# Optimization experiments

Measured on AMD Instinct MI355X. Metric: run time of the kernel, lower is better.

The kernel has to match this reference:

```python
import jax, jax.numpy as jnp
import numpy as np

N_NODES = 50000
N_EDGES = 800000
N_GRAPHS = 64
NEG_SLOPE = 0.2
EPS = 1e-16


def _gat_layer(x, src, dst, W, b, att_l, att_r):
    H, C = att_l.shape
    n = x.shape[0]
    # lin_l == lin_r (shared weights in the source module)
    xl = (x @ W.T + b).reshape(n, H, C)            # [N,H,C]
    alpha_l = jnp.sum(xl * att_l, axis=-1)         # [N,H]
    alpha_r = jnp.sum(xl * att_r, axis=-1)         # [N,H]
    # per-edge attention logits: alpha_i (dst) + alpha_j (src)
    e = jax.nn.leaky_relu(alpha_r[dst] + alpha_l[src], NEG_SLOPE)  # [E,H]
    # segment softmax over destination node
    m = jax.ops.segment_max(e, dst, num_segments=n)
    e = jnp.exp(e - m[dst])
    denom = jax.ops.segment_sum(e, dst, num_segments=n)
    alpha = e / (denom[dst] + EPS)                 # [E,H]
    msg = xl[src] * alpha[:, :, None]              # [E,H,C]
    out = jax.ops.segment_sum(msg, dst, num_segments=n)  # [N,H,C]
    return out.reshape(n, H * C)


def setup_inputs() -> dict:
    key = jax.random.key(0)
    ks = jax.random.split(key, 10)
    x = jax.random.normal(ks[0], (N_NODES, 128), dtype=jnp.float32)
    edge_index = jax.random.randint(ks[1], (2, N_EDGES), 0, N_NODES, dtype=jnp.int32)
    batch = jnp.sort(jax.random.randint(ks[2], (N_NODES,), 0, N_GRAPHS, dtype=jnp.int32))
    s = 1.0 / np.sqrt(128.0)
    Ws = jax.random.normal(ks[3], (3, 128, 128), dtype=jnp.float32) * s
    bs = jnp.zeros((3, 128), dtype=jnp.float32)
    att_ls = jax.random.normal(ks[4], (3, 4, 32), dtype=jnp.float32) * s
    att_rs = jax.random.normal(ks[5], (3, 4, 32), dtype=jnp.float32) * s
    proj_W = jax.random.normal(ks[6], (32, 128), dtype=jnp.float32) * s
    proj_b = jnp.zeros((32,), dtype=jnp.float32)
    return {"x": x, "edge_index": edge_index, "batch": batch, "Ws": Ws, "bs": bs,
            "att_ls": att_ls, "att_rs": att_rs, "proj_W": proj_W, "proj_b": proj_b}


def reference(x, edge_index, batch, Ws, bs, att_ls, att_rs, proj_W, proj_b):
    src, dst = edge_index[0], edge_index[1]
    h = x
    for l in range(3):
        h = _gat_layer(h, src, dst, Ws[l], bs[l], att_ls[l], att_rs[l])
        h = jax.nn.relu(h)  # dropout disabled (eval mode)
    pooled = jax.ops.segment_sum(h, batch, num_segments=N_GRAPHS)  # [G, H*C]
    return pooled @ proj_W.T + proj_b  # output_dim=None -> return embedding
```

## Files before the change

kernel.cpp:

```cpp
#include <hip/hip_runtime.h>
#include <hip/hip_bf16.h>

#define NHEADS 4
#define DIM 128
#define NEG_SLOPE 0.2f
#define POOL_CHUNK 256

typedef __bf16 bf16x8 __attribute__((ext_vector_type(8)));
typedef float  f32x4  __attribute__((ext_vector_type(4)));

__device__ __forceinline__ float lrelu(float x) { return x > 0.f ? x : NEG_SLOPE * x; }
__device__ __forceinline__ float bf2f(unsigned short u) {
    return __uint_as_float(((unsigned)u) << 16);
}
__device__ __forceinline__ unsigned short f2bf(float f) {
    __bf16 b = (__bf16)f;
    return __builtin_bit_cast(unsigned short, b);
}
__device__ __forceinline__ float4 lrelu4(float4 a, float4 b) {
    return make_float4(lrelu(a.x + b.x), lrelu(a.y + b.y), lrelu(a.z + b.z), lrelu(a.w + b.w));
}
__device__ __forceinline__ float4 redmax4(float4 v) {
#pragma unroll
    for (int off = 32; off >= 1; off >>= 1) {
        v.x = fmaxf(v.x, __shfl_xor(v.x, off));
        v.y = fmaxf(v.y, __shfl_xor(v.y, off));
        v.z = fmaxf(v.z, __shfl_xor(v.z, off));
        v.w = fmaxf(v.w, __shfl_xor(v.w, off));
    }
    return v;
}
__device__ __forceinline__ float4 redsum4(float4 v) {
#pragma unroll
    for (int off = 32; off >= 1; off >>= 1) {
        v.x += __shfl_xor(v.x, off);
        v.y += __shfl_xor(v.y, off);
        v.z += __shfl_xor(v.z, off);
        v.w += __shfl_xor(v.w, off);
    }
    return v;
}

__global__ __launch_bounds__(256) void pack_w(
    const float* __restrict__ Ws, __bf16* __restrict__ Wb, int total)
{
    int o = blockIdx.x * 256 + threadIdx.x;
    if (o >= total) return;
    int layer = o >> 14;
    int t = o & 16383;
    int j = t & 7, l = (t >> 3) & 63, kk = (t >> 9) & 3, g = t >> 11;
    int col = g * 16 + (l & 15);
    int k = kk * 32 + (l >> 4) * 8 + j;
    Wb[o] = (__bf16)Ws[(size_t)layer * 16384 + col * 128 + k];
}

template<bool ABF>
__device__ __forceinline__ void gemm_body(
    const float* __restrict__ inF, const unsigned short* __restrict__ inB,
    const uint4* __restrict__ Wb4, const float* __restrict__ bias,
    const float* __restrict__ attl, const float* __restrict__ attr,
    __bf16* __restrict__ xlb, float* __restrict__ al, float* __restrict__ ar,
    int n, int bid)
{
    const int tid = threadIdx.x;
    const int wid = tid >> 6, l = tid & 63;
    const int rowA = bid * 64 + wid * 16 + (l & 15);
    const int kchunk = (l >> 4) * 8;

    f32x4 acc[8];
#pragma unroll
    for (int g = 0; g < 8; ++g)
#pragma unroll
        for (int r = 0; r < 4; ++r) acc[g][r] = 0.f;

#pragma unroll
    for (int kk = 0; kk < 4; ++kk) {
        bf16x8 afrag;
        if (ABF) {
            uint4 u = make_uint4(0, 0, 0, 0);
            if (rowA < n)
                u = *(const uint4*)(inB + (size_t)rowA * DIM + kk * 32 + kchunk);
            afrag = __builtin_bit_cast(bf16x8, u);
        } else {
            float av[8];
            if (rowA < n) {
                const float* p = inF + (size_t)rowA * DIM + kk * 32 + kchunk;
                float4 x0 = *(const float4*)p;
                float4 x1 = *(const float4*)(p + 4);
                av[0]=x0.x; av[1]=x0.y; av[2]=x0.z; av[3]=x0.w;
                av[4]=x1.x; av[5]=x1.y; av[6]=x1.z; av[7]=x1.w;
            } else {
#pragma unroll
                for (int i = 0; i < 8; ++i) av[i] = 0.f;
            }
#pragma unroll
            for (int i = 0; i < 8; ++i) afrag[i] = (__bf16)av[i];
        }
#pragma unroll
        for (int g = 0; g < 8; ++g) {
            uint4 u = Wb4[(g * 4 + kk) * 64 + l];
            bf16x8 bfrag = __builtin_bit_cast(bf16x8, u);
            acc[g] = __builtin_amdgcn_mfma_f32_16x16x32_bf16(afrag, bfrag, acc[g], 0, 0, 0);
        }
    }

    const int rowbase = bid * 64 + wid * 16 + (l >> 4) * 4;
    float pl[4][4], pr2[4][4];
#pragma unroll
    for (int r = 0; r < 4; ++r)
#pragma unroll
        for (int h = 0; h < 4; ++h) { pl[r][h] = 0.f; pr2[r][h] = 0.f; }

#pragma unroll
    for (int g = 0; g < 8; ++g) {
        int col = g * 16 + (l & 15);
        float bg = bias[col], alg = attl[col], arg = attr[col];
        int h = g >> 1;
#pragma unroll
        for (int r = 0; r < 4; ++r) {
            float v = acc[g][r] + bg;
            int row = rowbase + r;
            if (row < n) xlb[(size_t)row * DIM + col] = (__bf16)v;
            pl[r][h]  = fmaf(v, alg, pl[r][h]);
            pr2[r][h] = fmaf(v, arg, pr2[r][h]);
        }
    }
#pragma unroll
    for (int off = 1; off <= 8; off <<= 1) {
#pragma unroll
        for (int r = 0; r < 4; ++r)
#pragma unroll
            for (int h = 0; h < 4; ++h) {
                pl[r][h]  += __shfl_xor(pl[r][h], off);
                pr2[r][h] += __shfl_xor(pr2[r][h], off);
            }
    }
    if ((l & 15) == 0) {
#pragma unroll
        for (int r = 0; r < 4; ++r) {
            int row = rowbase + r;
            if (row < n) {
#pragma unroll
                for (int h = 0; h < 4; ++h) {
                    al[row * 4 + h] = pl[r][h];
                    ar[row * 4 + h] = pr2[r][h];
                }
            }
        }
    }
}

template<bool ABF>
__global__ __launch_bounds__(256) void gemm_mfma(
    const float* __restrict__ inF, const unsigned short* __restrict__ inB,
    const uint4* __restrict__ Wb4, const float* __restrict__ bias,
    const float* __restrict__ attl, const float* __restrict__ attr,
    __bf16* __restrict__ xlb, float* __restrict__ al, float* __restrict__ ar, int n)
{
    gemm_body<ABF>(inF, inB, Wb4, bias, attl, attr, xlb, al, ar, n, blockIdx.x);
}

__global__ __launch_bounds__(256) void gemm0_scatter(
    const float* __restrict__ inF, const uint4* __restrict__ Wb4,
    const float* __restrict__ bias,
    const float* __restrict__ attl, const float* __restrict__ attr,
    __bf16* __restrict__ xlb, float* __restrict__ al, float* __restrict__ ar,
    int n, int gemmBlocks,
    const int* __restrict__ src, const int* __restrict__ dst,
    int* __restrict__ wpos, int* __restrict__ col, int E)
{
    if ((int)blockIdx.x < gemmBlocks) {
        gemm_body<false>(inF, nullptr, Wb4, bias, attl, attr, xlb, al, ar, n, blockIdx.x);
    } else {
        int e = (blockIdx.x - gemmBlocks) * 256 + threadIdx.x;
        if (e < E) {
            int p = atomicAdd(&wpos[dst[e]], 1);
            col[p] = src[e];
        }
    }
}

__global__ __launch_bounds__(256) void deg_count(
    const int* __restrict__ dst, int* __restrict__ deg, int E)
{
    int e = blockIdx.x * blockDim.x + threadIdx.x;
    if (e < E) atomicAdd(&deg[dst[e]], 1);
}

__global__ __launch_bounds__(256) void scan_blocks(
    const int* __restrict__ deg, int* __restrict__ rowptr,
    int* __restrict__ partials, int n)
{
    __shared__ int tot[256];
    int t = threadIdx.x;
    int base = blockIdx.x * 1024 + t * 4;
    int v[4];
#pragma unroll
    for (int j = 0; j < 4; ++j) v[j] = (base + j < n) ? deg[base + j] : 0;
    int p1 = v[0], p2 = p1 + v[1], p3 = p2 + v[2], sum4 = p3 + v[3];
    tot[t] = sum4;
    __syncthreads();
    int val = sum4;
    for (int off = 1; off < 256; off <<= 1) {
        int other = (t >= off) ? tot[t - off] : 0;
        __syncthreads();
        val += other;
        tot[t] = val;
        __syncthreads();
    }
    int excl = val - sum4;
    if (base < n)     rowptr[base]     = excl;
    if (base+1 < n)   rowptr[base+1]   = excl + p1;
    if (base+2 < n)   rowptr[base+2]   = excl + p2;
    if (base+3 < n)   rowptr[base+3]   = excl + p3;
    if (t == 255) partials[blockIdx.x] = val;
}

__global__ __launch_bounds__(256) void scan_partials(
    int* __restrict__ partials, int nb, int* __restrict__ rowptr, int n)
{
    __shared__ int tot[256];
    int t = threadIdx.x;
    int v = (t < nb) ? partials[t] : 0;
    tot[t] = v;
    __syncthreads();
    int val = v;
    for (int off = 1; off < 256; off <<= 1) {
        int other = (t >= off) ? tot[t - off] : 0;
        __syncthreads();
        val += other;
        tot[t] = val;
        __syncthreads();
    }
    if (t < nb) partials[t] = val - v;
    if (t == 255) rowptr[n] = val;
}

__global__ __launch_bounds__(256) void add_offsets(
    int* __restrict__ rowptr, int* __restrict__ wpos,
    const int* __restrict__ partials, int n)
{
    int base = blockIdx.x * 1024 + threadIdx.x * 4;
    int off = partials[blockIdx.x];
#pragma unroll
    for (int j = 0; j < 4; ++j) {
        int i = base + j;
        if (i < n) { int r = rowptr[i] + off; rowptr[i] = r; wpos[i] = r; }
    }
}

__device__ __forceinline__ void agg_chunk2(
    const int* __restrict__ slds, const float* __restrict__ wl,
    int cn, int q, const unsigned short* __restrict__ xp,
    f32x4& A, f32x4& B, f32x4& C, f32x4& D)
{
    int i = 0;
    for (; i + 8 <= cn; i += 8) {
        int e0 = i + q, e1 = i + 2 + q, e2 = i + 4 + q, e3 = i + 6 + q;
        int s0 = slds[e0], s1 = slds[e1], s2 = slds[e2], s3 = slds[e3];
        float w0 = wl[e0*4], w1 = wl[e1*4], w2 = wl[e2*4], w3 = wl[e3*4];
        ushort4 v0 = *(const ushort4*)(xp + (size_t)s0 * DIM);
        ushort4 v1 = *(const ushort4*)(xp + (size_t)s1 * DIM);
        ushort4 v2 = *(const ushort4*)(xp + (size_t)s2 * DIM);
        ushort4 v3 = *(const ushort4*)(xp + (size_t)s3 * DIM);
        A[0] = fmaf(w0, bf2f(v0.x), A[0]); A[1] = fmaf(w0, bf2f(v0.y), A[1]);
        A[2] = fmaf(w0, bf2f(v0.z), A[2]); A[3] = fmaf(w0, bf2f(v0.w), A[3]);
        B[0] = fmaf(w1, bf2f(v1.x), B[0]); B[1] = fmaf(w1, bf2f(v1.y), B[1]);
        B[2] = fmaf(w1, bf2f(v1.z), B[2]); B[3] = fmaf(w1, bf2f(v1.w), B[3]);
        C[0] = fmaf(w2, bf2f(v2.x), C[0]); C[1] = fmaf(w2, bf2f(v2.y), C[1]);
        C[2] = fmaf(w2, bf2f(v2.z), C[2]); C[3] = fmaf(w2, bf2f(v2.w), C[3]);
        D[0] = fmaf(w3, bf2f(v3.x), D[0]); D[1] = fmaf(w3, bf2f(v3.y), D[1]);
        D[2] = fmaf(w3, bf2f(v3.z), D[2]); D[3] = fmaf(w3, bf2f(v3.w), D[3]);
    }
    for (; i < cn; i += 2) {
        int e = i + q;
        if (e < cn) {
            int s = slds[e];
            float w = wl[e*4];
            ushort4 v = *(const ushort4*)(xp + (size_t)s * DIM);
            A[0] = fmaf(w, bf2f(v.x), A[0]); A[1] = fmaf(w, bf2f(v.y), A[1]);
            A[2] = fmaf(w, bf2f(v.z), A[2]); A[3] = fmaf(w, bf2f(v.w), A[3]);
        }
    }
}

__global__ __launch_bounds__(256) void gat_aggregate(
    const int* __restrict__ rowptr, const int* __restrict__ col,
    const float* __restrict__ al, const float* __restrict__ ar,
    const unsigned short* __restrict__ xlb, unsigned short* __restrict__ outb, int n)
{
    __shared__ float4 wlds[4][64];
    __shared__ int    slds[4][64];
    int wid = threadIdx.x >> 6;
    int node = blockIdx.x * 4 + wid;
    if (node >= n) return;
    int lane = threadIdx.x & 63;
    int q = lane >> 5, c32 = lane & 31;
    int h = c32 >> 3;
    int r0 = rowptr[node], r1 = rowptr[node + 1];
    int deg = r1 - r0;
    unsigned short* po = outb + (size_t)node * DIM + c32 * 4;
    if (deg == 0) {
        if (q == 0) *(ushort4*)po = make_ushort4(0, 0, 0, 0);
        return;
    }

    float4 arv = *(const float4*)(ar + (size_t)node * 4);
    const float* wl = (const float*)&wlds[wid][0] + h;
    const unsigned short* xp = xlb + c32 * 4;
    f32x4 A = {0.f,0.f,0.f,0.f}, B = {0.f,0.f,0.f,0.f};
    f32x4 C = {0.f,0.f,0.f,0.f}, D = {0.f,0.f,0.f,0.f};
    float4 inv4;

    if (deg <= 64) {
        float4 l4 = make_float4(-1e30f, -1e30f, -1e30f, -1e30f);
        int s = 0;
        if (lane < deg) {
            s = col[r0 + lane];
            float4 a = *(const float4*)(al + (size_t)s * 4);
            l4 = lrelu4(arv, a);
        }
        float4 m4 = redmax4(l4);
        float4 p4 = make_float4(0.f, 0.f, 0.f, 0.f);
        if (lane < deg) {
            p4.x = __expf(l4.x - m4.x); p4.y = __expf(l4.y - m4.y);
            p4.z = __expf(l4.z - m4.z); p4.w = __expf(l4.w - m4.w);
        }
        float4 s4 = redsum4(p4);
        inv4 = make_float4(1.f/(s4.x+1e-16f), 1.f/(s4.y+1e-16f),
                           1.f/(s4.z+1e-16f), 1.f/(s4.w+1e-16f));
        if (lane < deg) { wlds[wid][lane] = p4; slds[wid][lane] = s; }
        __asm__ volatile("s_waitcnt lgkmcnt(0)" ::: "memory");
        __builtin_amdgcn_sched_barrier(0);
        agg_chunk2(&slds[wid][0], wl, deg, q, xp, A, B, C, D);
    } else {
        float4 m4 = make_float4(-1e30f, -1e30f, -1e30f, -1e30f);
        for (int i = lane; i < deg; i += 64) {
            int s = col[r0 + i];
            float4 a = *(const float4*)(al + (size_t)s * 4);
            float4 t = lrelu4(arv, a);
            m4.x = fmaxf(m4.x, t.x); m4.y = fmaxf(m4.y, t.y);
            m4.z = fmaxf(m4.z, t.z); m4.w = fmaxf(m4.w, t.w);
        }
        m4 = redmax4(m4);
        float4 s4 = make_float4(0.f, 0.f, 0.f, 0.f);
        for (int i = lane; i < deg; i += 64) {
            int s = col[r0 + i];
            float4 a = *(const float4*)(al + (size_t)s * 4);
            float4 t = lrelu4(arv, a);
            s4.x += __expf(t.x - m4.x); s4.y += __expf(t.y - m4.y);
            s4.z += __expf(t.z - m4.z); s4.w += __expf(t.w - m4.w);
        }
        s4 = redsum4(s4);
        inv4 = make_float4(1.f/(s4.x+1e-16f), 1.f/(s4.y+1e-16f),
                           1.f/(s4.z+1e-16f), 1.f/(s4.w+1e-16f));
        for (int c0 = 0; c0 < deg; c0 += 64) {
            int cn = min(64, deg - c0);
            if (lane < cn) {
                int s = col[r0 + c0 + lane];
                float4 a = *(const float4*)(al + (size_t)s * 4);
                float4 t = lrelu4(arv, a);
                float4 p;
                p.x = __expf(t.x - m4.x); p.y = __expf(t.y - m4.y);
                p.z = __expf(t.z - m4.z); p.w = __expf(t.w - m4.w);
                wlds[wid][lane] = p; slds[wid][lane] = s;
            }
            __asm__ volatile("s_waitcnt lgkmcnt(0)" ::: "memory");
            __builtin_amdgcn_sched_barrier(0);
            agg_chunk2(&slds[wid][0], wl, cn, q, xp, A, B, C, D);
            __asm__ volatile("s_waitcnt lgkmcnt(0)" ::: "memory");
            __builtin_amdgcn_sched_barrier(0);
        }
    }
    float invh = (h == 0) ? inv4.x : (h == 1) ? inv4.y : (h == 2) ? inv4.z : inv4.w;
    f32x4 T;
#pragma unroll
    for (int j = 0; j < 4; ++j) {
        T[j] = A[j] + B[j] + C[j] + D[j];
        T[j] += __shfl_xor(T[j], 32);
    }
    if (q == 0) {
        ushort4 o4;
        o4.x = f2bf(fmaxf(T[0] * invh, 0.f));
        o4.y = f2bf(fmaxf(T[1] * invh, 0.f));
        o4.z = f2bf(fmaxf(T[2] * invh, 0.f));
        o4.w = f2bf(fmaxf(T[3] * invh, 0.f));
        *(ushort4*)po = o4;
    }
}

__global__ __launch_bounds__(256) void pool_nodes_seg(
    const unsigned short* __restrict__ h, const int* __restrict__ batch,
    float* __restrict__ pooled, int n)
{
    int wid = threadIdx.x >> 6;
    int lane = threadIdx.x & 63;
    int start = blockIdx.x * POOL_CHUNK;
    int end = min(start + POOL_CHUNK, n);
    float a0 = 0.f, a1 = 0.f;
    int curg = -1;
    for (int node = start + wid; node < end; node += 4) {
        int g = batch[node];
        if (g != curg) {
            if (curg >= 0) {
                unsafeAtomicAdd(pooled + (size_t)curg * DIM + lane*2,     a0);
                unsafeAtomicAdd(pooled + (size_t)curg * DIM + lane*2 + 1, a1);
            }
            curg = g; a0 = 0.f; a1 = 0.f;
        }
        ushort2 v = *(const ushort2*)(h + (size_t)node * DIM + lane * 2);
        a0 += bf2f(v.x);
        a1 += bf2f(v.y);
    }
    if (curg >= 0) {
        unsafeAtomicAdd(pooled + (size_t)curg * DIM + lane*2,     a0);
        unsafeAtomicAdd(pooled + (size_t)curg * DIM + lane*2 + 1, a1);
    }
}

__global__ __launch_bounds__(256) void proj_out(
    const float* __restrict__ pooled, const float* __restrict__ W,
    const float* __restrict__ b, float* __restrict__ out, int G)
{
    int idx = blockIdx.x * blockDim.x + threadIdx.x;
    if (idx >= G * 32) return;
    int g = idx >> 5, j = idx & 31;
    const float* pr = pooled + (size_t)g * DIM;
    const float* wr = W + (size_t)j * DIM;
    float acc = 0.f;
#pragma unroll
    for (int k = 0; k < DIM; ++k) acc = fmaf(pr[k], wr[k], acc);
    out[idx] = acc + b[j];
}

extern "C" void kernel_launch(void* const* d_in, const int* in_sizes, int n_in,
                              void* d_out, int out_size, void* d_ws, size_t ws_size,
                              hipStream_t stream)
{
    const float* x      = (const float*)d_in[0];
    const int*   eidx   = (const int*)d_in[1];
    const int*   batch  = (const int*)d_in[2];
    const float* Ws     = (const float*)d_in[3];
    const float* bs     = (const float*)d_in[4];
    const float* attls  = (const float*)d_in[5];
    const float* attrs  = (const float*)d_in[6];
    const float* projW  = (const float*)d_in[7];
    const float* projb  = (const float*)d_in[8];

    const int N = in_sizes[0] / DIM;
    const int E = in_sizes[1] / 2;
    const int G = out_size / 32;
    const int* src = eidx;
    const int* dst = eidx + E;

    char* ws = (char*)d_ws;
    size_t o = 0;
    auto alloc = [&](size_t bytes) { char* p = ws + o; o += (bytes + 255) & ~255ull; return p; };
    unsigned short* hA  = (unsigned short*)alloc((size_t)N * DIM * 2);
    unsigned short* hB  = (unsigned short*)alloc((size_t)N * DIM * 2);
    __bf16* xlb    = (__bf16*)alloc((size_t)N * DIM * 2);
    float*  al     = (float*)alloc((size_t)N * 4 * 4);
    float*  ar     = (float*)alloc((size_t)N * 4 * 4);
    int*    rowptr = (int*)alloc((size_t)(N + 1) * 4);
    int*    wpos   = (int*)alloc((size_t)N * 4);
    int*    deg    = (int*)alloc((size_t)N * 4);
    int*    colv   = (int*)alloc((size_t)E * 4);
    int*    parts  = (int*)alloc(256 * 4);
    float*  pooled = (float*)alloc((size_t)G * DIM * 4);
    __bf16* Wb     = (__bf16*)alloc((size_t)3 * 16384 * 2);

    const int wtot = 3 * 16384;
    pack_w<<<(wtot + 255) / 256, 256, 0, stream>>>(Ws, Wb, wtot);

    const int nb = (N + 1023) / 1024;
    hipMemsetAsync(deg, 0, (size_t)N * 4, stream);
    deg_count<<<(E + 255) / 256, 256, 0, stream>>>(dst, deg, E);
    scan_blocks<<<nb, 256, 0, stream>>>(deg, rowptr, parts, N);
    scan_partials<<<1, 256, 0, stream>>>(parts, nb, rowptr, N);
    add_offsets<<<nb, 256, 0, stream>>>(rowptr, wpos, parts, N);

    const int gb = (N + 63) / 64;
    const int sb = (E + 255) / 256;

    gemm0_scatter<<<gb + sb, 256, 0, stream>>>(
        x, (const uint4*)Wb, bs, attls, attrs, xlb, al, ar, N, gb,
        src, dst, wpos, colv, E);
    gat_aggregate<<<(N + 3) / 4, 256, 0, stream>>>(rowptr, colv, al, ar,
        (const unsigned short*)xlb, hA, N);

    const unsigned short* hin = hA;
    unsigned short* houts[2] = {hB, hA};
    for (int l = 1; l < 3; ++l) {
        unsigned short* hout = houts[l - 1];
        const uint4* Wb4 = (const uint4*)(Wb + (size_t)l * 16384);
        gemm_mfma<true><<<gb, 256, 0, stream>>>(nullptr, hin, Wb4, bs + l*DIM,
            attls + l*DIM, attrs + l*DIM, xlb, al, ar, N);
        gat_aggregate<<<(N + 3) / 4, 256, 0, stream>>>(rowptr, colv, al, ar,
            (const unsigned short*)xlb, hout, N);
        hin = hout;
    }

    hipMemsetAsync(pooled, 0, (size_t)G * DIM * 4, stream);
    pool_nodes_seg<<<(N + POOL_CHUNK - 1) / POOL_CHUNK, 256, 0, stream>>>(hA, batch, pooled, N);
    proj_out<<<(G * 32 + 255) / 256, 256, 0, stream>>>(pooled, projW, projb, (float*)d_out, G);
}
```

Before: 319.5 us.

## Split GAT aggregation into edge-softmax kernel and per-head gather kernel

The fused softmax-plus-aggregate kernel is split in two. One kernel computes normalized per-edge attention weights and stores them in bf16 per-head planes. A second gather kernel launches one block per head for each pair of node groups, with each wave handling a node's 32 channels for a single head, so head-adjacent blocks share cached source rows. This adds an extra launch plus write/read traffic for the edge weights, and stores the weights in bf16, in exchange for a narrower, more parallel gather with better L2 locality.

```diff
diff --git a/kernel.cpp b/kernel.cpp
--- a/kernel.cpp
+++ b/kernel.cpp
@@ -249,74 +249,24 @@
     }
 }
 
-__device__ __forceinline__ void agg_chunk2(
-    const int* __restrict__ slds, const float* __restrict__ wl,
-    int cn, int q, const unsigned short* __restrict__ xp,
-    f32x4& A, f32x4& B, f32x4& C, f32x4& D)
-{
-    int i = 0;
-    for (; i + 8 <= cn; i += 8) {
-        int e0 = i + q, e1 = i + 2 + q, e2 = i + 4 + q, e3 = i + 6 + q;
-        int s0 = slds[e0], s1 = slds[e1], s2 = slds[e2], s3 = slds[e3];
-        float w0 = wl[e0*4], w1 = wl[e1*4], w2 = wl[e2*4], w3 = wl[e3*4];
-        ushort4 v0 = *(const ushort4*)(xp + (size_t)s0 * DIM);
-        ushort4 v1 = *(const ushort4*)(xp + (size_t)s1 * DIM);
-        ushort4 v2 = *(const ushort4*)(xp + (size_t)s2 * DIM);
-        ushort4 v3 = *(const ushort4*)(xp + (size_t)s3 * DIM);
-        A[0] = fmaf(w0, bf2f(v0.x), A[0]); A[1] = fmaf(w0, bf2f(v0.y), A[1]);
-        A[2] = fmaf(w0, bf2f(v0.z), A[2]); A[3] = fmaf(w0, bf2f(v0.w), A[3]);
-        B[0] = fmaf(w1, bf2f(v1.x), B[0]); B[1] = fmaf(w1, bf2f(v1.y), B[1]);
-        B[2] = fmaf(w1, bf2f(v1.z), B[2]); B[3] = fmaf(w1, bf2f(v1.w), B[3]);
-        C[0] = fmaf(w2, bf2f(v2.x), C[0]); C[1] = fmaf(w2, bf2f(v2.y), C[1]);
-        C[2] = fmaf(w2, bf2f(v2.z), C[2]); C[3] = fmaf(w2, bf2f(v2.w), C[3]);
-        D[0] = fmaf(w3, bf2f(v3.x), D[0]); D[1] = fmaf(w3, bf2f(v3.y), D[1]);
-        D[2] = fmaf(w3, bf2f(v3.z), D[2]); D[3] = fmaf(w3, bf2f(v3.w), D[3]);
-    }
-    for (; i < cn; i += 2) {
-        int e = i + q;
-        if (e < cn) {
-            int s = slds[e];
-            float w = wl[e*4];
-            ushort4 v = *(const ushort4*)(xp + (size_t)s * DIM);
-            A[0] = fmaf(w, bf2f(v.x), A[0]); A[1] = fmaf(w, bf2f(v.y), A[1]);
-            A[2] = fmaf(w, bf2f(v.z), A[2]); A[3] = fmaf(w, bf2f(v.w), A[3]);
-        }
-    }
-}
-
-__global__ __launch_bounds__(256) void gat_aggregate(
+__global__ __launch_bounds__(256) void edge_softmax(
     const int* __restrict__ rowptr, const int* __restrict__ col,
     const float* __restrict__ al, const float* __restrict__ ar,
-    const unsigned short* __restrict__ xlb, unsigned short* __restrict__ outb, int n)
-{
-    __shared__ float4 wlds[4][64];
-    __shared__ int    slds[4][64];
-    int wid = threadIdx.x >> 6;
-    int node = blockIdx.x * 4 + wid;
+    unsigned short* __restrict__ wcsr, int n, int E)
+{
+    int node = blockIdx.x * 4 + (threadIdx.x >> 6);
     if (node >= n) return;
     int lane = threadIdx.x & 63;
-    int q = lane >> 5, c32 = lane & 31;
-    int h = c32 >> 3;
     int r0 = rowptr[node], r1 = rowptr[node + 1];
     int deg = r1 - r0;
-    unsigned short* po = outb + (size_t)node * DIM + c32 * 4;
-    if (deg == 0) {
-        if (q == 0) *(ushort4*)po = make_ushort4(0, 0, 0, 0);
-        return;
-    }
+    if (deg == 0) return;
 
     float4 arv = *(const float4*)(ar + (size_t)node * 4);
-    const float* wl = (const float*)&wlds[wid][0] + h;
-    const unsigned short* xp = xlb + c32 * 4;
-    f32x4 A = {0.f,0.f,0.f,0.f}, B = {0.f,0.f,0.f,0.f};
-    f32x4 C = {0.f,0.f,0.f,0.f}, D = {0.f,0.f,0.f,0.f};
-    float4 inv4;
 
     if (deg <= 64) {
         float4 l4 = make_float4(-1e30f, -1e30f, -1e30f, -1e30f);
-        int s = 0;
         if (lane < deg) {
-            s = col[r0 + lane];
+            int s = col[r0 + lane];
             float4 a = *(const float4*)(al + (size_t)s * 4);
             l4 = lrelu4(arv, a);
         }
@@ -327,12 +277,13 @@
             p4.z = __expf(l4.z - m4.z); p4.w = __expf(l4.w - m4.w);
         }
         float4 s4 = redsum4(p4);
-        inv4 = make_float4(1.f/(s4.x+1e-16f), 1.f/(s4.y+1e-16f),
-                           1.f/(s4.z+1e-16f), 1.f/(s4.w+1e-16f));
-        if (lane < deg) { wlds[wid][lane] = p4; slds[wid][lane] = s; }
-        __asm__ volatile("s_waitcnt lgkmcnt(0)" ::: "memory");
-        __builtin_amdgcn_sched_barrier(0);
-        agg_chunk2(&slds[wid][0], wl, deg, q, xp, A, B, C, D);
+        if (lane < deg) {
+            size_t base = (size_t)(r0 + lane);
+            wcsr[base]             = f2bf(p4.x / (s4.x + 1e-16f));
+            wcsr[(size_t)E + base]   = f2bf(p4.y / (s4.y + 1e-16f));
+            wcsr[(size_t)2*E + base] = f2bf(p4.z / (s4.z + 1e-16f));
+            wcsr[(size_t)3*E + base] = f2bf(p4.w / (s4.w + 1e-16f));
+        }
     } else {
         float4 m4 = make_float4(-1e30f, -1e30f, -1e30f, -1e30f);
         for (int i = lane; i < deg; i += 64) {
@@ -352,40 +303,89 @@
             s4.z += __expf(t.z - m4.z); s4.w += __expf(t.w - m4.w);
         }
         s4 = redsum4(s4);
-        inv4 = make_float4(1.f/(s4.x+1e-16f), 1.f/(s4.y+1e-16f),
-                           1.f/(s4.z+1e-16f), 1.f/(s4.w+1e-16f));
-        for (int c0 = 0; c0 < deg; c0 += 64) {
-            int cn = min(64, deg - c0);
-            if (lane < cn) {
-                int s = col[r0 + c0 + lane];
-                float4 a = *(const float4*)(al + (size_t)s * 4);
-                float4 t = lrelu4(arv, a);
-                float4 p;
-                p.x = __expf(t.x - m4.x); p.y = __expf(t.y - m4.y);
-                p.z = __expf(t.z - m4.z); p.w = __expf(t.w - m4.w);
-                wlds[wid][lane] = p; slds[wid][lane] = s;
+        float4 inv4 = make_float4(1.f/(s4.x+1e-16f), 1.f/(s4.y+1e-16f),
+                                  1.f/(s4.z+1e-16f), 1.f/(s4.w+1e-16f));
+        for (int i = lane; i < deg; i += 64) {
+            int s = col[r0 + i];
+            float4 a = *(const float4*)(al + (size_t)s * 4);
+            float4 t = lrelu4(arv, a);
+            size_t base = (size_t)(r0 + i);
+            wcsr[base]               = f2bf(__expf(t.x - m4.x) * inv4.x);
+            wcsr[(size_t)E + base]   = f2bf(__expf(t.y - m4.y) * inv4.y);
+            wcsr[(size_t)2*E + base] = f2bf(__expf(t.z - m4.z) * inv4.z);
+            wcsr[(size_t)3*E + base] = f2bf(__expf(t.w - m4.w) * inv4.w);
+        }
+    }
+}
+
+__global__ __launch_bounds__(256) void gat_gather(
+    const int* __restrict__ rowptr, const int* __restrict__ col,
+    const unsigned short* __restrict__ wcsr, const unsigned short* __restrict__ xlb,
+    unsigned short* __restrict__ outb, int n, int E, int NB)
+{
+    __shared__ int    sle[4][64];
+    __shared__ unsigned short wle[4][64];
+    int x = blockIdx.x & 7;
+    int h = x & 3;
+    int g = (blockIdx.x >> 3) * 2 + (x >> 2);
+    if (g >= NB) return;
+    int wid = threadIdx.x >> 6;
+    int node = g * 4 + wid;
+    if (node >= n) return;
+    int lane = threadIdx.x & 63;
+    int eg = lane >> 4, c16 = lane & 15;
+    int r0 = rowptr[node], r1 = rowptr[node + 1];
+    int deg = r1 - r0;
+    unsigned short* po = outb + (size_t)node * DIM + h * 32 + c16 * 2;
+    if (deg == 0) {
+        if (eg == 0) *(ushort2*)po = make_ushort2(0, 0);
+        return;
+    }
+    const unsigned short* wplane = wcsr + (size_t)h * E;
+    const unsigned short* xp = xlb + h * 32 + c16 * 2;
+
+    float a0 = 0.f, a1 = 0.f, b0 = 0.f, b1 = 0.f;
+    for (int c0 = 0; c0 < deg; c0 += 64) {
+        int cn = min(64, deg - c0);
+        if (lane < cn) {
+            sle[wid][lane] = col[r0 + c0 + lane];
+            wle[wid][lane] = wplane[r0 + c0 + lane];
+        }
+        __asm__ volatile("s_waitcnt lgkmcnt(0)" ::: "memory");
+        __builtin_amdgcn_sched_barrier(0);
+        int i = 0;
+        for (; i + 8 <= cn; i += 8) {
+            int e0 = i + eg, e1 = i + 4 + eg;
+            int s0 = sle[wid][e0], s1 = sle[wid][e1];
+            float w0 = bf2f(wle[wid][e0]), w1 = bf2f(wle[wid][e1]);
+            unsigned v0 = *(const unsigned*)(xp + (size_t)s0 * DIM);
+            unsigned v1 = *(const unsigned*)(xp + (size_t)s1 * DIM);
+            a0 = fmaf(w0, __uint_as_float(v0 << 16), a0);
+            a1 = fmaf(w0, __uint_as_float(v0 & 0xffff0000u), a1);
+            b0 = fmaf(w1, __uint_as_float(v1 << 16), b0);
+            b1 = fmaf(w1, __uint_as_float(v1 & 0xffff0000u), b1);
+        }
+        for (; i < cn; i += 4) {
+            int e = i + eg;
+            if (e < cn) {
+                int s = sle[wid][e];
+                float w = bf2f(wle[wid][e]);
+                unsigned v = *(const unsigned*)(xp + (size_t)s * DIM);
+                a0 = fmaf(w, __uint_as_float(v << 16), a0);
+                a1 = fmaf(w, __uint_as_float(v & 0xffff0000u), a1);
             }
-            __asm__ volatile("s_waitcnt lgkmcnt(0)" ::: "memory");
-            __builtin_amdgcn_sched_barrier(0);
-            agg_chunk2(&slds[wid][0], wl, cn, q, xp, A, B, C, D);
-            __asm__ volatile("s_waitcnt lgkmcnt(0)" ::: "memory");
-            __builtin_amdgcn_sched_barrier(0);
-        }
-    }
-    float invh = (h == 0) ? inv4.x : (h == 1) ? inv4.y : (h == 2) ? inv4.z : inv4.w;
-    f32x4 T;
-#pragma unroll
-    for (int j = 0; j < 4; ++j) {
-        T[j] = A[j] + B[j] + C[j] + D[j];
-        T[j] += __shfl_xor(T[j], 32);
-    }
-    if (q == 0) {
-        ushort4 o4;
-        o4.x = f2bf(fmaxf(T[0] * invh, 0.f));
-        o4.y = f2bf(fmaxf(T[1] * invh, 0.f));
-        o4.z = f2bf(fmaxf(T[2] * invh, 0.f));
-        o4.w = f2bf(fmaxf(T[3] * invh, 0.f));
-        *(ushort4*)po = o4;
+        }
+        __asm__ volatile("s_waitcnt lgkmcnt(0)" ::: "memory");
+        __builtin_amdgcn_sched_barrier(0);
+    }
+    a0 += b0; a1 += b1;
+    a0 += __shfl_xor(a0, 16); a0 += __shfl_xor(a0, 32);
+    a1 += __shfl_xor(a1, 16); a1 += __shfl_xor(a1, 32);
+    if (eg == 0) {
+        ushort2 o2;
+        o2.x = f2bf(fmaxf(a0, 0.f));
+        o2.y = f2bf(fmaxf(a1, 0.f));
+        *(ushort2*)po = o2;
     }
 }
 
@@ -465,6 +465,7 @@
     int*    wpos   = (int*)alloc((size_t)N * 4);
     int*    deg    = (int*)alloc((size_t)N * 4);
     int*    colv   = (int*)alloc((size_t)E * 4);
+    unsigned short* wcsr = (unsigned short*)alloc((size_t)4 * E * 2);
     int*    parts  = (int*)alloc(256 * 4);
     float*  pooled = (float*)alloc((size_t)G * DIM * 4);
     __bf16* Wb     = (__bf16*)alloc((size_t)3 * 16384 * 2);
@@ -481,12 +482,15 @@
 
     const int gb = (N + 63) / 64;
     const int sb = (E + 255) / 256;
+    const int NB = (N + 3) / 4;
+    const int gatherGrid = ((NB + 1) / 2) * 8;
 
     gemm0_scatter<<<gb + sb, 256, 0, stream>>>(
         x, (const uint4*)Wb, bs, attls, attrs, xlb, al, ar, N, gb,
         src, dst, wpos, colv, E);
-    gat_aggregate<<<(N + 3) / 4, 256, 0, stream>>>(rowptr, colv, al, ar,
-        (const unsigned short*)xlb, hA, N);
+    edge_softmax<<<NB, 256, 0, stream>>>(rowptr, colv, al, ar, wcsr, N, E);
+    gat_gather<<<gatherGrid, 256, 0, stream>>>(rowptr, colv, wcsr,
+        (const unsigned short*)xlb, hA, N, E, NB);
 
     const unsigned short* hin = hA;
     unsigned short* houts[2] = {hB, hA};
@@ -495,8 +499,9 @@
         const uint4* Wb4 = (const uint4*)(Wb + (size_t)l * 16384);
         gemm_mfma<true><<<gb, 256, 0, stream>>>(nullptr, hin, Wb4, bs + l*DIM,
             attls + l*DIM, attrs + l*DIM, xlb, al, ar, N);
-        gat_aggregate<<<(N + 3) / 4, 256, 0, stream>>>(rowptr, colv, al, ar,
-            (const unsigned short*)xlb, hout, N);
+        edge_softmax<<<NB, 256, 0, stream>>>(rowptr, colv, al, ar, wcsr, N, E);
+        gat_gather<<<gatherGrid, 256, 0, stream>>>(rowptr, colv, wcsr,
+            (const unsigned short*)xlb, hout, N, E, NB);
         hin = hout;
     }
 
```

Result: slower. 470.8 us (+47.4%).

## Build CSR columns with bucketed two-pass LDS sort instead of global atomics

Applied to the files above, without the earlier changes.

The old per-edge global atomicAdd scatter into the CSR column array is replaced. Edges are first classified into 256-node destination buckets per 4096-edge block using an LDS histogram and scan, then written to a bucket-ordered buffer. A second kernel ranks edges within each bucket using LDS atomics. This removes random global atomics and scattered writes but adds an extra kernel and buffer pass. It also assumes node ids fit in 16 bits and the bucket count fits in 256.

```diff
diff --git a/kernel.cpp b/kernel.cpp
--- a/kernel.cpp
+++ b/kernel.cpp
@@ -160,23 +160,76 @@
     gemm_body<ABF>(inF, inB, Wb4, bias, attl, attr, xlb, al, ar, n, blockIdx.x);
 }
 
-__global__ __launch_bounds__(256) void gemm0_scatter(
+__global__ __launch_bounds__(256) void gemm0_classify(
     const float* __restrict__ inF, const uint4* __restrict__ Wb4,
     const float* __restrict__ bias,
     const float* __restrict__ attl, const float* __restrict__ attr,
     __bf16* __restrict__ xlb, float* __restrict__ al, float* __restrict__ ar,
     int n, int gemmBlocks,
     const int* __restrict__ src, const int* __restrict__ dst,
-    int* __restrict__ wpos, int* __restrict__ col, int E)
+    int* __restrict__ bwpos, unsigned* __restrict__ ebuf, int E)
 {
     if ((int)blockIdx.x < gemmBlocks) {
         gemm_body<false>(inF, nullptr, Wb4, bias, attl, attr, xlb, al, ar, n, blockIdx.x);
     } else {
-        int e = (blockIdx.x - gemmBlocks) * 256 + threadIdx.x;
-        if (e < E) {
-            int p = atomicAdd(&wpos[dst[e]], 1);
-            col[p] = src[e];
-        }
+        __shared__ unsigned stage[4096];
+        __shared__ unsigned char sid[4096];
+        __shared__ int hist[256], lofs[256], wofs[256], gbase[256];
+        int t = threadIdx.x;
+        int e0 = (blockIdx.x - gemmBlocks) * 4096;
+        int cnt = min(4096, E - e0);
+        if (cnt <= 0) return;
+        hist[t] = 0;
+        __syncthreads();
+        for (int k = t; k < cnt; k += 256)
+            atomicAdd(&hist[dst[e0 + k] >> 8], 1);
+        __syncthreads();
+        int v = hist[t];
+        lofs[t] = v;
+        __syncthreads();
+        int val = v;
+        for (int off = 1; off < 256; off <<= 1) {
+            int other = (t >= off) ? lofs[t - off] : 0;
+            __syncthreads();
+            val += other;
+            lofs[t] = val;
+            __syncthreads();
+        }
+        int excl = val - v;
+        int gb_ = (v > 0) ? atomicAdd(&bwpos[t], v) : 0;
+        lofs[t] = excl; wofs[t] = excl; gbase[t] = gb_;
+        __syncthreads();
+        for (int k = t; k < cnt; k += 256) {
+            int d = dst[e0 + k], s = src[e0 + k];
+            int b = d >> 8;
+            int slot = atomicAdd(&wofs[b], 1);
+            stage[slot] = (unsigned)(s & 0xffff) | ((unsigned)(d & 255) << 16);
+            sid[slot] = (unsigned char)b;
+        }
+        __syncthreads();
+        for (int s_ = t; s_ < cnt; s_ += 256) {
+            int b = sid[s_];
+            ebuf[gbase[b] + (s_ - lofs[b])] = stage[s_];
+        }
+    }
+}
+
+__global__ __launch_bounds__(256) void bucket_rank(
+    const unsigned* __restrict__ ebuf, const int* __restrict__ rowptr,
+    int* __restrict__ col, int n)
+{
+    __shared__ int wp[256];
+    int nb0 = blockIdx.x << 8;
+    int t = threadIdx.x;
+    int nend = min(nb0 + 256, n);
+    int base = rowptr[nb0];
+    int eend = rowptr[nend];
+    if (nb0 + t < nend) wp[t] = rowptr[nb0 + t] - base;
+    __syncthreads();
+    for (int e = base + t; e < eend; e += 256) {
+        unsigned ed = ebuf[e];
+        int r = atomicAdd(&wp[(ed >> 16) & 255], 1);
+        col[base + r] = (int)(ed & 0xffffu);
     }
 }
 
@@ -237,7 +290,7 @@
 }
 
 __global__ __launch_bounds__(256) void add_offsets(
-    int* __restrict__ rowptr, int* __restrict__ wpos,
+    int* __restrict__ rowptr, int* __restrict__ bwpos,
     const int* __restrict__ partials, int n)
 {
     int base = blockIdx.x * 1024 + threadIdx.x * 4;
@@ -245,7 +298,11 @@
 #pragma unroll
     for (int j = 0; j < 4; ++j) {
         int i = base + j;
-        if (i < n) { int r = rowptr[i] + off; rowptr[i] = r; wpos[i] = r; }
+        if (i < n) {
+            int r = rowptr[i] + off;
+            rowptr[i] = r;
+            if ((i & 255) == 0) bwpos[i >> 8] = r;
+        }
     }
 }
 
@@ -462,9 +519,10 @@
     float*  al     = (float*)alloc((size_t)N * 4 * 4);
     float*  ar     = (float*)alloc((size_t)N * 4 * 4);
     int*    rowptr = (int*)alloc((size_t)(N + 1) * 4);
-    int*    wpos   = (int*)alloc((size_t)N * 4);
     int*    deg    = (int*)alloc((size_t)N * 4);
     int*    colv   = (int*)alloc((size_t)E * 4);
+    unsigned* ebuf = (unsigned*)alloc((size_t)E * 4);
+    int*    bwpos  = (int*)alloc((size_t)((N + 255) / 256) * 4);
     int*    parts  = (int*)alloc(256 * 4);
     float*  pooled = (float*)alloc((size_t)G * DIM * 4);
     __bf16* Wb     = (__bf16*)alloc((size_t)3 * 16384 * 2);
@@ -477,14 +535,16 @@
     deg_count<<<(E + 255) / 256, 256, 0, stream>>>(dst, deg, E);
     scan_blocks<<<nb, 256, 0, stream>>>(deg, rowptr, parts, N);
     scan_partials<<<1, 256, 0, stream>>>(parts, nb, rowptr, N);
-    add_offsets<<<nb, 256, 0, stream>>>(rowptr, wpos, parts, N);
+    add_offsets<<<nb, 256, 0, stream>>>(rowptr, bwpos, parts, N);
 
     const int gb = (N + 63) / 64;
-    const int sb = (E + 255) / 256;
-
-    gemm0_scatter<<<gb + sb, 256, 0, stream>>>(
+    const int cb = (E + 4095) / 4096;
+    const int rb = (N + 255) / 256;
+
+    gemm0_classify<<<gb + cb, 256, 0, stream>>>(
         x, (const uint4*)Wb, bs, attls, attrs, xlb, al, ar, N, gb,
-        src, dst, wpos, colv, E);
+        src, dst, bwpos, ebuf, E);
+    bucket_rank<<<rb, 256, 0, stream>>>(ebuf, rowptr, colv, N);
     gat_aggregate<<<(N + 3) / 4, 256, 0, stream>>>(rowptr, colv, al, ar,
         (const unsigned short*)xlb, hA, N);
 
```

Result: faster. 293.3 us (-8.2%).
